# Performance work log

Hardware: AMD Instinct MI355X
Metric: run time of the kernel (lower is better)

## Reference

```python
import jax, jax.numpy as jnp
import numpy as np


def setup_inputs() -> dict:
    key = jax.random.key(0)
    k1, k2 = jax.random.split(key)
    B, Q, T, D = 128, 512, 512, 256
    inputs = jax.random.normal(k1, (B, T, D), dtype=jnp.float32)
    query = jax.random.normal(k2, (B, Q, D), dtype=jnp.float32)
    return {"inputs": inputs, "query": query}


def reference(inputs, query):
    # inputs: [B, T, D] (keys == values), query: [B, Q, D]
    D = inputs.shape[2]
    scale = 1.0 / jnp.sqrt(jnp.asarray(D, dtype=inputs.dtype))
    # scores: [B, Q, T]
    scores = jnp.einsum("bqd,btd->bqt", query, inputs) * scale
    weights = jax.nn.softmax(scores, axis=2)
    # attended: [B, Q, D]
    attended = jnp.einsum("bqt,btd->bqd", weights, inputs)
    # pool over query dim -> [B, D]
    return jnp.sum(attended, axis=1)
```

## Files before the change

kernel.cpp:

```cpp
#include <hip/hip_runtime.h>
#include <hip/hip_bf16.h>


typedef __bf16 bf16x8 __attribute__((ext_vector_type(8)));
typedef float  f32x4  __attribute__((ext_vector_type(4)));

#define B_    128
#define Tn    512
#define Dn    256
#define SCALE 0.0625f

__device__ __forceinline__ int lidx(int row, int ch) {
  return row * 256 + (((ch ^ (row & 31)) & 31) << 3);
}

__device__ __forceinline__ void kload(const float* __restrict__ src, int tid,
                                      float4* pre) {
#pragma unroll
  for (int i = 0; i < 4; ++i) {
    int u = i * 512 + tid;
    int row = u >> 5, ch = u & 31;
    const float4* p = (const float4*)(src + row * 256 + ch * 8);
    pre[2 * i]     = p[0];
    pre[2 * i + 1] = p[1];
  }
}

__device__ __forceinline__ void kstore(__bf16* dst, int tid,
                                       const float4* pre) {
#pragma unroll
  for (int i = 0; i < 4; ++i) {
    int u = i * 512 + tid;
    int row = u >> 5, ch = u & 31;
    float4 v0 = pre[2 * i], v1 = pre[2 * i + 1];
    bf16x8 w;
    w[0] = (__bf16)v0.x; w[1] = (__bf16)v0.y;
    w[2] = (__bf16)v0.z; w[3] = (__bf16)v0.w;
    w[4] = (__bf16)v1.x; w[5] = (__bf16)v1.y;
    w[6] = (__bf16)v1.z; w[7] = (__bf16)v1.w;
    *(bf16x8*)(dst + lidx(row, ch)) = w;
  }
}

__global__ void __launch_bounds__(512, 2) attn_qk(
    const float* __restrict__ inputs, const float* __restrict__ query,
    float* __restrict__ c_tot) {
  __shared__ __bf16 Qs[128 * 256];
  __shared__ __bf16 Ks[2][64 * 256];

  const int tid  = threadIdx.x;
  const int bidx = blockIdx.x;
  const int b  = bidx & 127;
  const int qt = bidx >> 7;

  const float* qsrc = query  + ((size_t)b * 512 + (size_t)qt * 128) * Dn;
  const float* ksrc = inputs + (size_t)b * Tn * Dn;

  const int wave = tid >> 6, lane = tid & 63;
  const int quad = lane >> 4, l15 = lane & 15;
  const int qg = wave >> 1;
  const int th = wave & 1;

#pragma unroll
  for (int i = 0; i < 8; ++i) {
    int u = i * 512 + tid;
    int row = u >> 5, ch = u & 31;
    const float4* p = (const float4*)(qsrc + row * 256 + ch * 8);
    float4 v0 = p[0], v1 = p[1];
    bf16x8 w;
    w[0] = (__bf16)v0.x; w[1] = (__bf16)v0.y;
    w[2] = (__bf16)v0.z; w[3] = (__bf16)v0.w;
    w[4] = (__bf16)v1.x; w[5] = (__bf16)v1.y;
    w[6] = (__bf16)v1.z; w[7] = (__bf16)v1.w;
    *(bf16x8*)(Qs + lidx(row, ch)) = w;
  }

  float4 pre[8];
  kload(ksrc, tid, pre);
  __syncthreads();

  bf16x8 afrag[2][8];
#pragma unroll
  for (int m = 0; m < 2; ++m)
#pragma unroll
    for (int dc = 0; dc < 8; ++dc)
      afrag[m][dc] =
          *(const bf16x8*)(Qs + lidx(qg * 32 + m * 16 + l15, dc * 4 + quad));

  kstore(Ks[0], tid, pre);
  __syncthreads();

  f32x4 acc[8][2][2];
  f32x4 zero = {0.f, 0.f, 0.f, 0.f};
#pragma unroll
  for (int tt = 0; tt < 8; ++tt)
#pragma unroll
    for (int ct = 0; ct < 2; ++ct) {
      acc[tt][ct][0] = zero;
      acc[tt][ct][1] = zero;
    }

#pragma unroll
  for (int tt = 0; tt < 8; ++tt) {
    if (tt < 7) kload(ksrc + (size_t)(tt + 1) * 64 * Dn, tid, pre);
    const __bf16* cur = Ks[tt & 1];
#pragma unroll
    for (int dc = 0; dc < 8; ++dc) {
#pragma unroll
      for (int ct = 0; ct < 2; ++ct) {
        bf16x8 bb =
            *(const bf16x8*)(cur + lidx(th * 32 + ct * 16 + l15, dc * 4 + quad));
        acc[tt][ct][0] = __builtin_amdgcn_mfma_f32_16x16x32_bf16(
            afrag[0][dc], bb, acc[tt][ct][0], 0, 0, 0);
        acc[tt][ct][1] = __builtin_amdgcn_mfma_f32_16x16x32_bf16(
            afrag[1][dc], bb, acc[tt][ct][1], 0, 0, 0);
      }
    }
    if (tt < 7) kstore((__bf16*)Ks[(tt + 1) & 1], tid, pre);
    __syncthreads();
  }

  float* lred  = (float*)Ks[0];
  float* cpart = (float*)Ks[0] + 256;

  float rs[2][4];
#pragma unroll
  for (int m = 0; m < 2; ++m)
#pragma unroll
    for (int r = 0; r < 4; ++r) rs[m][r] = 0.f;
#pragma unroll
  for (int tt = 0; tt < 8; ++tt)
#pragma unroll
    for (int ct = 0; ct < 2; ++ct)
#pragma unroll
      for (int m = 0; m < 2; ++m)
#pragma unroll
        for (int r = 0; r < 4; ++r) {
          float p = __expf(acc[tt][ct][m][r] * SCALE);
          acc[tt][ct][m][r] = p;
          rs[m][r] += p;
        }
#pragma unroll
  for (int off = 1; off <= 8; off <<= 1)
#pragma unroll
    for (int m = 0; m < 2; ++m)
#pragma unroll
      for (int r = 0; r < 4; ++r) rs[m][r] += __shfl_xor(rs[m][r], off);

  if (l15 == 0) {
#pragma unroll
    for (int m = 0; m < 2; ++m)
#pragma unroll
      for (int r = 0; r < 4; ++r)
        lred[(qg * 2 + th) * 32 + m * 16 + quad * 4 + r] = rs[m][r];
  }
  __syncthreads();

  float linv[2][4];
#pragma unroll
  for (int m = 0; m < 2; ++m)
#pragma unroll
    for (int r = 0; r < 4; ++r) {
      int row = m * 16 + quad * 4 + r;
      linv[m][r] =
          1.f / (lred[(qg * 2 + 0) * 32 + row] + lred[(qg * 2 + 1) * 32 + row]);
    }

#pragma unroll
  for (int tt = 0; tt < 8; ++tt)
#pragma unroll
    for (int ct = 0; ct < 2; ++ct) {
      float v = 0.f;
#pragma unroll
      for (int m = 0; m < 2; ++m)
#pragma unroll
        for (int r = 0; r < 4; ++r) v += acc[tt][ct][m][r] * linv[m][r];
      v += __shfl_xor(v, 16);
      v += __shfl_xor(v, 32);
      if (quad == 0)
        cpart[qg * 512 + tt * 64 + th * 32 + ct * 16 + l15] = v;
    }
  __syncthreads();

  float c = cpart[tid] + cpart[512 + tid] + cpart[1024 + tid] + cpart[1536 + tid];
  atomicAdd(c_tot + (size_t)b * Tn + tid, c);
}

__global__ void __launch_bounds__(256) attn_av(
    const float* __restrict__ inputs, const float* __restrict__ c_tot,
    float* __restrict__ out) {
  __shared__ float cs[64];
  __shared__ float psum[3][256];
  const int bid = blockIdx.x, tid = threadIdx.x;
  const int b = bid & 127, sl = bid >> 7;

  if (tid < 64) cs[tid] = c_tot[(size_t)b * Tn + sl * 64 + tid];
  __syncthreads();

  const int w = tid >> 6, d4 = tid & 63;
  const float4* vb =
      (const float4*)(inputs + ((size_t)b * Tn + sl * 64 + w * 16) * Dn) + d4;
  float ox = 0.f, oy = 0.f, oz = 0.f, ow = 0.f;
#pragma unroll
  for (int j = 0; j < 16; ++j) {
    float c = cs[w * 16 + j];
    float4 v = vb[(size_t)j * 64];
    ox += c * v.x; oy += c * v.y; oz += c * v.z; ow += c * v.w;
  }
  if (w) {
    float4 t = {ox, oy, oz, ow};
    *(float4*)&psum[w - 1][d4 * 4] = t;
  }
  __syncthreads();
  if (!w) {
    float4 p0 = *(float4*)&psum[0][d4 * 4];
    float4 p1 = *(float4*)&psum[1][d4 * 4];
    float4 p2 = *(float4*)&psum[2][d4 * 4];
    float* op = out + b * 256 + d4 * 4;
    atomicAdd(op + 0, ox + p0.x + p1.x + p2.x);
    atomicAdd(op + 1, oy + p0.y + p1.y + p2.y);
    atomicAdd(op + 2, oz + p0.z + p1.z + p2.z);
    atomicAdd(op + 3, ow + p0.w + p1.w + p2.w);
  }
}

extern "C" void kernel_launch(void* const* d_in, const int* in_sizes, int n_in,
                              void* d_out, int out_size, void* d_ws, size_t ws_size,
                              hipStream_t stream) {
  const float* inputs = (const float*)d_in[0];
  const float* query  = (const float*)d_in[1];
  float* out   = (float*)d_out;
  float* c_tot = (float*)d_ws;

  hipMemsetAsync(out, 0, (size_t)B_ * Dn * sizeof(float), stream);
  hipMemsetAsync(c_tot, 0, (size_t)B_ * Tn * sizeof(float), stream);
  attn_qk<<<dim3(512), dim3(512), 0, stream>>>(inputs, query, c_tot);
  attn_av<<<dim3(1024), dim3(256), 0, stream>>>(inputs, c_tot, out);
}
```

Measured before the change: 183.9 us.

## Deepen K prefetch pipeline, reload Q fragments from LDS, drop atomics

Key tiles are now prefetched two tiles ahead using two register buffers. Each tile is written to LDS at the start of the iteration that precedes its use, so global latency overlaps more compute. To pay for the extra prefetch registers, the Q fragments are no longer held in registers and are re-read from LDS in every dc step, which adds LDS traffic. The memset and atomicAdd on the per-token coefficient buffer are replaced by per-query-tile partial buffers that attn_av sums, which needs four times the workspace.

Result: faster. 179.1 us (-2.7%).

```diff
diff --git a/kernel.cpp b/kernel.cpp
--- a/kernel.cpp
+++ b/kernel.cpp
@@ -44,9 +44,10 @@
 
 __global__ void __launch_bounds__(512, 2) attn_qk(
     const float* __restrict__ inputs, const float* __restrict__ query,
-    float* __restrict__ c_tot) {
-  __shared__ __bf16 Qs[128 * 256];
-  __shared__ __bf16 Ks[2][64 * 256];
+    float* __restrict__ c_ws) {
+  __shared__ __bf16 smem[128 * 256 + 2 * 64 * 256];
+  __bf16* Qs = smem;
+  __bf16* Kb[2] = {smem + 128 * 256, smem + 128 * 256 + 64 * 256};
 
   const int tid  = threadIdx.x;
   const int bidx = blockIdx.x;
@@ -60,6 +61,10 @@
   const int quad = lane >> 4, l15 = lane & 15;
   const int qg = wave >> 1;
   const int th = wave & 1;
+
+  float4 pre[2][8];
+
+  kload(ksrc, tid, pre[0]);
 
 #pragma unroll
   for (int i = 0; i < 8; ++i) {
@@ -75,19 +80,11 @@
     *(bf16x8*)(Qs + lidx(row, ch)) = w;
   }
 
-  float4 pre[8];
-  kload(ksrc, tid, pre);
-  __syncthreads();
-
-  bf16x8 afrag[2][8];
-#pragma unroll
-  for (int m = 0; m < 2; ++m)
-#pragma unroll
-    for (int dc = 0; dc < 8; ++dc)
-      afrag[m][dc] =
-          *(const bf16x8*)(Qs + lidx(qg * 32 + m * 16 + l15, dc * 4 + quad));
-
-  kstore(Ks[0], tid, pre);
+  kload(ksrc + (size_t)1 * 64 * Dn, tid, pre[1]);
+  __syncthreads();
+
+  kstore(Kb[0], tid, pre[0]);
+  kload(ksrc + (size_t)2 * 64 * Dn, tid, pre[0]);
   __syncthreads();
 
   f32x4 acc[8][2][2];
@@ -102,26 +99,29 @@
 
 #pragma unroll
   for (int tt = 0; tt < 8; ++tt) {
-    if (tt < 7) kload(ksrc + (size_t)(tt + 1) * 64 * Dn, tid, pre);
-    const __bf16* cur = Ks[tt & 1];
+    if (tt < 7) kstore(Kb[(tt + 1) & 1], tid, pre[(tt + 1) & 1]);
+    if (tt < 5) kload(ksrc + (size_t)(tt + 3) * 64 * Dn, tid, pre[(tt + 1) & 1]);
+
+    const __bf16* cur = Kb[tt & 1];
 #pragma unroll
     for (int dc = 0; dc < 8; ++dc) {
+      bf16x8 a0 = *(const bf16x8*)(Qs + lidx(qg * 32 + l15, dc * 4 + quad));
+      bf16x8 a1 = *(const bf16x8*)(Qs + lidx(qg * 32 + 16 + l15, dc * 4 + quad));
 #pragma unroll
       for (int ct = 0; ct < 2; ++ct) {
         bf16x8 bb =
             *(const bf16x8*)(cur + lidx(th * 32 + ct * 16 + l15, dc * 4 + quad));
         acc[tt][ct][0] = __builtin_amdgcn_mfma_f32_16x16x32_bf16(
-            afrag[0][dc], bb, acc[tt][ct][0], 0, 0, 0);
+            a0, bb, acc[tt][ct][0], 0, 0, 0);
         acc[tt][ct][1] = __builtin_amdgcn_mfma_f32_16x16x32_bf16(
-            afrag[1][dc], bb, acc[tt][ct][1], 0, 0, 0);
+            a1, bb, acc[tt][ct][1], 0, 0, 0);
       }
     }
-    if (tt < 7) kstore((__bf16*)Ks[(tt + 1) & 1], tid, pre);
     __syncthreads();
   }
 
-  float* lred  = (float*)Ks[0];
-  float* cpart = (float*)Ks[0] + 256;
+  float* lred  = (float*)Kb[0];
+  float* cpart = (float*)Kb[0] + 256;
 
   float rs[2][4];
 #pragma unroll
@@ -182,19 +182,29 @@
     }
   __syncthreads();
 
-  float c = cpart[tid] + cpart[512 + tid] + cpart[1024 + tid] + cpart[1536 + tid];
-  atomicAdd(c_tot + (size_t)b * Tn + tid, c);
+  float* cout = c_ws + ((size_t)qt * B_ + b) * Tn;
+#pragma unroll
+  for (int t = tid; t < 512; t += 256) {
+    if (t < 512)
+      cout[t] = cpart[t] + cpart[512 + t] + cpart[1024 + t] + cpart[1536 + t];
+  }
 }
 
 __global__ void __launch_bounds__(256) attn_av(
-    const float* __restrict__ inputs, const float* __restrict__ c_tot,
+    const float* __restrict__ inputs, const float* __restrict__ c_ws,
     float* __restrict__ out) {
   __shared__ float cs[64];
   __shared__ float psum[3][256];
   const int bid = blockIdx.x, tid = threadIdx.x;
   const int b = bid & 127, sl = bid >> 7;
 
-  if (tid < 64) cs[tid] = c_tot[(size_t)b * Tn + sl * 64 + tid];
+  if (tid < 64) {
+    int t = sl * 64 + tid;
+    cs[tid] = c_ws[(size_t)(0 * B_ + b) * Tn + t] +
+              c_ws[(size_t)(1 * B_ + b) * Tn + t] +
+              c_ws[(size_t)(2 * B_ + b) * Tn + t] +
+              c_ws[(size_t)(3 * B_ + b) * Tn + t];
+  }
   __syncthreads();
 
   const int w = tid >> 6, d4 = tid & 63;
@@ -229,11 +239,10 @@
                               hipStream_t stream) {
   const float* inputs = (const float*)d_in[0];
   const float* query  = (const float*)d_in[1];
-  float* out   = (float*)d_out;
-  float* c_tot = (float*)d_ws;
+  float* out  = (float*)d_out;
+  float* c_ws = (float*)d_ws;
 
   hipMemsetAsync(out, 0, (size_t)B_ * Dn * sizeof(float), stream);
-  hipMemsetAsync(c_tot, 0, (size_t)B_ * Tn * sizeof(float), stream);
-  attn_qk<<<dim3(512), dim3(512), 0, stream>>>(inputs, query, c_tot);
-  attn_av<<<dim3(1024), dim3(256), 0, stream>>>(inputs, c_tot, out);
-}
+  attn_qk<<<dim3(512), dim3(512), 0, stream>>>(inputs, query, c_ws);
+  attn_av<<<dim3(1024), dim3(256), 0, stream>>>(inputs, c_ws, out);
+}
```
